# Optimization experiments

Measured on AMD Instinct MI355X. Metric: run time of the kernel, lower is better.

## Reference

```python
import jax, jax.numpy as jnp
import numpy as np

# HOG config (matches init_kwargs / skimage defaults for block_norm='L2-Hys')
ORIENTATIONS = 9
CELL = 8          # pixels_per_cell (square)
BLOCK = 2         # cells_per_block (square)
EPS = 1e-5        # skimage block-norm epsilon


def setup_inputs() -> dict:
    key = jax.random.key(0)
    x = jax.random.uniform(key, (64, 1, 512, 512), dtype=jnp.float32)
    return {"x": x}


def _hog(img):
    # img: (B, H, W) grayscale float
    B, H, W = img.shape
    # skimage _hog_channel_gradient: central differences, zero at borders
    g_row = jnp.zeros_like(img).at[:, 1:-1, :].set(img[:, 2:, :] - img[:, :-2, :])
    g_col = jnp.zeros_like(img).at[:, :, 1:-1].set(img[:, :, 2:] - img[:, :, :-2])
    mag = jnp.hypot(g_row, g_col)
    # unsigned orientation in [0, 180)
    ori = jnp.degrees(jnp.arctan2(g_row, g_col)) % 180.0
    bin_width = 180.0 / ORIENTATIONS
    bin_idx = jnp.minimum((ori / bin_width).astype(jnp.int32), ORIENTATIONS - 1)

    ncr, ncc = H // CELL, W // CELL  # number of cells per row/col
    mag_c = mag[:, : ncr * CELL, : ncc * CELL].reshape(B, ncr, CELL, ncc, CELL)
    bin_c = bin_idx[:, : ncr * CELL, : ncc * CELL].reshape(B, ncr, CELL, ncc, CELL)

    # per-cell orientation histogram; skimage averages by cell area
    hists = []
    for i in range(ORIENTATIONS):  # small fixed loop over 9 bins
        hists.append(jnp.where(bin_c == i, mag_c, 0.0).sum(axis=(2, 4)))
    hist = jnp.stack(hists, axis=-1) / (CELL * CELL)  # (B, ncr, ncc, O)

    # sliding blocks of BLOCK x BLOCK cells, stride 1 cell
    nbr, nbc = ncr - BLOCK + 1, ncc - BLOCK + 1
    tmp = jnp.stack([hist[:, br : br + nbr] for br in range(BLOCK)], axis=2)       # (B,nbr,BLOCK,ncc,O)
    blocks = jnp.stack([tmp[:, :, :, bc : bc + nbc] for bc in range(BLOCK)], axis=4)  # (B,nbr,BLOCK,nbc,BLOCK,O)
    blocks = blocks.transpose(0, 1, 3, 2, 4, 5)  # (B, nbr, nbc, BLOCK, BLOCK, O)

    # L2-Hys normalization (skimage default block_norm)
    n1 = jnp.sqrt(jnp.sum(blocks * blocks, axis=(-3, -2, -1), keepdims=True) + EPS**2)
    b = jnp.minimum(blocks / n1, 0.2)
    n2 = jnp.sqrt(jnp.sum(b * b, axis=(-3, -2, -1), keepdims=True) + EPS**2)
    normalized = b / n2
    return normalized.reshape(B, -1)  # feature_vector=True ravel per image


def reference(x):
    return _hog(x[:, 0, :, :].astype(jnp.float32))
```

## Files before the change

kernel.cpp:

```cpp
#include <hip/hip_runtime.h>


#define ORIENT 9
#define IMH 512
#define IMW 512
#define NCR 64
#define NCC 64
#define NBR 63
#define NBC 63
#define NIMG 64

__global__ __launch_bounds__(256) void hog_cell_hist(const float* __restrict__ img,
                                                     float* __restrict__ hist) {
    __shared__ float lh[32 * ORIENT];
    const int tx = threadIdx.x;
    const int ty = threadIdx.y;
    const int tid = ty * 32 + tx;

    lh[tid] = 0.f;
    if (tid < 32) lh[tid + 256] = 0.f;
    __syncthreads();

    const int c0 = blockIdx.x * 256 + tx * 8;
    const int r  = blockIdx.y * 8 + ty;
    const float* im = img + (size_t)blockIdx.z * (IMH * IMW) + (size_t)r * IMW + c0;

    const float4* imv = (const float4*)im;
    float4 a0 = imv[0], b0 = imv[1];
    float4 am = {0,0,0,0}, bm = {0,0,0,0};
    float4 ap = {0,0,0,0}, bp = {0,0,0,0};
    const bool rin = (r > 0) && (r < IMH - 1);
    if (r > 0)       { const float4* p = (const float4*)(im - IMW); am = p[0]; bm = p[1]; }
    if (r < IMH - 1) { const float4* p = (const float4*)(im + IMW); ap = p[0]; bp = p[1]; }
    const float left  = (c0 > 0)       ? im[-1] : 0.f;
    const float right = (c0 + 8 < IMW) ? im[8]  : 0.f;

    float rv[10] = {left, a0.x, a0.y, a0.z, a0.w, b0.x, b0.y, b0.z, b0.w, right};
    float pv[8]  = {ap.x, ap.y, ap.z, ap.w, bp.x, bp.y, bp.z, bp.w};
    float mv[8]  = {am.x, am.y, am.z, am.w, bm.x, bm.y, bm.z, bm.w};

    float* cellh = &lh[tx * ORIENT];
#pragma unroll
    for (int j = 0; j < 8; ++j) {
        const float gr = rin ? (pv[j] - mv[j]) : 0.f;
        const bool cin = (c0 + j > 0) && (c0 + j < IMW - 1);
        const float gc = cin ? (rv[j + 2] - rv[j]) : 0.f;
        const float mag = sqrtf(gr * gr + gc * gc);
        float ori = atan2f(gr, gc) * 57.29577951308232f;
        ori = (ori >= 180.0f) ? ori - 180.0f : ori;
        ori = (ori <   0.0f) ? ori + 180.0f : ori;
        int bin = (int)(ori / 20.0f);
        bin = bin > (ORIENT - 1) ? (ORIENT - 1) : bin;
        atomicAdd(&cellh[bin], mag);
    }
    __syncthreads();

    float* hrow = hist + (((size_t)blockIdx.z * NCR + blockIdx.y) * NCC + blockIdx.x * 32) * ORIENT;
    hrow[tid] = lh[tid] * (1.f / 64.f);
    if (tid < 32) hrow[tid + 256] = lh[tid + 256] * (1.f / 64.f);
}

__global__ __launch_bounds__(256) void hog_block_norm(const float* __restrict__ hist,
                                                      float* __restrict__ out) {
    const int total = NIMG * NBR * NBC;
    int t = blockIdx.x * blockDim.x + threadIdx.x;
    if (t >= total) return;

    const int bc = t % NBC;
    const int br = (t / NBC) % NBR;
    const int b  = t / (NBC * NBR);

    float v[36];
    float s = 0.f;
#pragma unroll
    for (int i = 0; i < 2; ++i) {
        const float* row = hist + (((size_t)b * NCR + br + i) * NCC + bc) * ORIENT;
#pragma unroll
        for (int k = 0; k < 18; ++k) { float h = row[k]; v[i * 18 + k] = h; s += h * h; }
    }
    const float r1 = 1.0f / sqrtf(s + 1e-10f);
    float s2 = 0.f;
#pragma unroll
    for (int k = 0; k < 36; ++k) {
        float x = fminf(v[k] * r1, 0.2f);
        v[k] = x;
        s2 += x * x;
    }
    const float r2 = 1.0f / sqrtf(s2 + 1e-10f);

    float4* o = (float4*)(out + (size_t)t * 36);
#pragma unroll
    for (int k = 0; k < 9; ++k)
        o[k] = make_float4(v[4*k] * r2, v[4*k+1] * r2, v[4*k+2] * r2, v[4*k+3] * r2);
}

extern "C" void kernel_launch(void* const* d_in, const int* in_sizes, int n_in,
                              void* d_out, int out_size, void* d_ws, size_t ws_size,
                              hipStream_t stream) {
    const float* x = (const float*)d_in[0];
    float* out  = (float*)d_out;
    float* hist = (float*)d_ws;

    dim3 b1(32, 8, 1);
    dim3 g1(IMW / 256, IMH / 8, NIMG);
    hipLaunchKernelGGL(hog_cell_hist, g1, b1, 0, stream, x, hist);

    const int total = NIMG * NBR * NBC;
    dim3 b2(256, 1, 1);
    dim3 g2((total + 255) / 256, 1, 1);
    hipLaunchKernelGGL(hog_block_norm, g2, b2, 0, stream, hist, out);
}
```

Before: 188.4 us.

## Stage block-norm histogram rows in shared memory and batch histogram atomics

The block-normalisation kernel now runs one 64-thread workgroup per block row and image. It copies the two needed histogram rows into shared memory with coalesced float4 loads, so threads no longer make strided global reads of overlapping cells. The cell-histogram kernel computes all eight magnitudes and bins first, then does the LDS atomics in a separate loop, and it gains a min-blocks hint in its launch bounds. One thread per workgroup idles in the norm kernel, and the small workgroups may lower occupancy.

```diff
diff --git a/kernel.cpp b/kernel.cpp
--- a/kernel.cpp
+++ b/kernel.cpp
@@ -10,8 +10,8 @@
 #define NBC 63
 #define NIMG 64
 
-__global__ __launch_bounds__(256) void hog_cell_hist(const float* __restrict__ img,
-                                                     float* __restrict__ hist) {
+__global__ __launch_bounds__(256, 4) void hog_cell_hist(const float* __restrict__ img,
+                                                        float* __restrict__ hist) {
     __shared__ float lh[32 * ORIENT];
     const int tx = threadIdx.x;
     const int ty = threadIdx.y;
@@ -39,20 +39,23 @@
     float pv[8]  = {ap.x, ap.y, ap.z, ap.w, bp.x, bp.y, bp.z, bp.w};
     float mv[8]  = {am.x, am.y, am.z, am.w, bm.x, bm.y, bm.z, bm.w};
 
-    float* cellh = &lh[tx * ORIENT];
+    float mags[8];
+    int   bins[8];
 #pragma unroll
     for (int j = 0; j < 8; ++j) {
         const float gr = rin ? (pv[j] - mv[j]) : 0.f;
         const bool cin = (c0 + j > 0) && (c0 + j < IMW - 1);
         const float gc = cin ? (rv[j + 2] - rv[j]) : 0.f;
-        const float mag = sqrtf(gr * gr + gc * gc);
+        mags[j] = sqrtf(gr * gr + gc * gc);
         float ori = atan2f(gr, gc) * 57.29577951308232f;
         ori = (ori >= 180.0f) ? ori - 180.0f : ori;
         ori = (ori <   0.0f) ? ori + 180.0f : ori;
         int bin = (int)(ori / 20.0f);
-        bin = bin > (ORIENT - 1) ? (ORIENT - 1) : bin;
-        atomicAdd(&cellh[bin], mag);
+        bins[j] = bin > (ORIENT - 1) ? (ORIENT - 1) : bin;
     }
+    float* cellh = &lh[tx * ORIENT];
+#pragma unroll
+    for (int j = 0; j < 8; ++j) atomicAdd(&cellh[bins[j]], mags[j]);
     __syncthreads();
 
     float* hrow = hist + (((size_t)blockIdx.z * NCR + blockIdx.y) * NCC + blockIdx.x * 32) * ORIENT;
@@ -60,24 +63,32 @@
     if (tid < 32) hrow[tid + 256] = lh[tid + 256] * (1.f / 64.f);
 }
 
-__global__ __launch_bounds__(256) void hog_block_norm(const float* __restrict__ hist,
-                                                      float* __restrict__ out) {
-    const int total = NIMG * NBR * NBC;
-    int t = blockIdx.x * blockDim.x + threadIdx.x;
-    if (t >= total) return;
+__global__ __launch_bounds__(64) void hog_block_norm(const float* __restrict__ hist,
+                                                     float* __restrict__ out) {
+    __shared__ float lh[2 * NCC * ORIENT];
+    const int tid = threadIdx.x;
+    const int br  = blockIdx.x;
+    const int b   = blockIdx.y;
 
-    const int bc = t % NBC;
-    const int br = (t / NBC) % NBR;
-    const int b  = t / (NBC * NBR);
+    const float4* src = (const float4*)(hist + ((size_t)b * NCR + br) * (NCC * ORIENT));
+    float4* dst = (float4*)lh;
+#pragma unroll
+    for (int k = 0; k < 5; ++k) {
+        int idx = k * 64 + tid;
+        if (idx < 288) dst[idx] = src[idx];
+    }
+    __syncthreads();
+
+    const int bc = tid;
+    if (bc >= NBC) return;
 
     float v[36];
     float s = 0.f;
 #pragma unroll
-    for (int i = 0; i < 2; ++i) {
-        const float* row = hist + (((size_t)b * NCR + br + i) * NCC + bc) * ORIENT;
+    for (int k = 0; k < 18; ++k) { float h = lh[bc * ORIENT + k];               v[k]      = h; s += h * h; }
 #pragma unroll
-        for (int k = 0; k < 18; ++k) { float h = row[k]; v[i * 18 + k] = h; s += h * h; }
-    }
+    for (int k = 0; k < 18; ++k) { float h = lh[NCC * ORIENT + bc * ORIENT + k]; v[18 + k] = h; s += h * h; }
+
     const float r1 = 1.0f / sqrtf(s + 1e-10f);
     float s2 = 0.f;
 #pragma unroll
@@ -88,7 +99,7 @@
     }
     const float r2 = 1.0f / sqrtf(s2 + 1e-10f);
 
-    float4* o = (float4*)(out + (size_t)t * 36);
+    float4* o = (float4*)(out + (((size_t)b * NBR + br) * NBC + bc) * 36);
 #pragma unroll
     for (int k = 0; k < 9; ++k)
         o[k] = make_float4(v[4*k] * r2, v[4*k+1] * r2, v[4*k+2] * r2, v[4*k+3] * r2);
@@ -105,8 +116,7 @@
     dim3 g1(IMW / 256, IMH / 8, NIMG);
     hipLaunchKernelGGL(hog_cell_hist, g1, b1, 0, stream, x, hist);
 
-    const int total = NIMG * NBR * NBC;
-    dim3 b2(256, 1, 1);
-    dim3 g2((total + 255) / 256, 1, 1);
+    dim3 b2(64, 1, 1);
+    dim3 g2(NBR, NIMG, 1);
     hipLaunchKernelGGL(hog_block_norm, g2, b2, 0, stream, hist, out);
 }
```

Result: slower. 195.0 us (+3.5%).
